# Performance work log

Hardware: AMD Instinct MI355X
Metric: run time of the kernel (lower is better)

The kernel has to match this reference:

```python
import jax, jax.numpy as jnp
import numpy as np

N_NODES = 100000
NEG_SLOPE = 0.2


def _gat_conv(x, edge_index, W, att_src, att_dst, bias):
    """Single-head PyG-style GATConv with self-loops.
    x: [N, F_in], edge_index: [2, E] (row 0 = src j, row 1 = dst i).
    """
    N = x.shape[0]
    h = x @ W  # [N, F_out]
    # add self-loops
    loop = jnp.arange(N, dtype=edge_index.dtype)
    src = jnp.concatenate([edge_index[0], loop])
    dst = jnp.concatenate([edge_index[1], loop])
    # per-node attention terms, gathered per edge
    a_s = h @ att_src  # [N]
    a_d = h @ att_dst  # [N]
    e = jax.nn.leaky_relu(a_s[src] + a_d[dst], NEG_SLOPE)  # [E+N]
    # segment softmax over incoming edges of each destination
    m = jax.ops.segment_max(e, dst, num_segments=N)  # [N]
    m = jnp.where(jnp.isfinite(m), m, 0.0)
    p = jnp.exp(e - m[dst])
    denom = jax.ops.segment_sum(p, dst, num_segments=N)  # [N], >0 due to self-loops
    alpha = p / denom[dst]  # [E+N]
    # scatter-aggregate weighted source features
    out = jax.ops.segment_sum(h[src] * alpha[:, None], dst, num_segments=N)
    return out + bias


def setup_inputs() -> dict:
    key = jax.random.key(0)
    ks = jax.random.split(key, 12)
    F_in, H, C = 128, 64, 40
    x = jax.random.normal(ks[0], (N_NODES, F_in), dtype=jnp.float32)
    edge_index = jax.random.randint(ks[1], (2, 1600000), 0, N_NODES, dtype=jnp.int64)
    s1 = 1.0 / np.sqrt(F_in)
    s2 = 1.0 / np.sqrt(H)
    return {
        "x": x,
        "edge_index": edge_index,
        "W1": jax.random.uniform(ks[2], (F_in, H), jnp.float32, -s1, s1),
        "att_src1": jax.random.uniform(ks[3], (H,), jnp.float32, -s2, s2),
        "att_dst1": jax.random.uniform(ks[4], (H,), jnp.float32, -s2, s2),
        "b1": jnp.zeros((H,), jnp.float32),
        "W2": jax.random.uniform(ks[5], (H, C), jnp.float32, -s2, s2),
        "att_src2": jax.random.uniform(ks[6], (C,), jnp.float32, -1.0 / np.sqrt(C), 1.0 / np.sqrt(C)),
        "att_dst2": jax.random.uniform(ks[7], (C,), jnp.float32, -1.0 / np.sqrt(C), 1.0 / np.sqrt(C)),
        "b2": jnp.zeros((C,), jnp.float32),
    }


def reference(x, edge_index, W1, att_src1, att_dst1, b1, W2, att_src2, att_dst2, b2):
    h = _gat_conv(x, edge_index, W1, att_src1, att_dst1, b1)
    h = jax.nn.relu(h)
    # dropout is identity in eval mode
    out = _gat_conv(h, edge_index, W2, att_src2, att_dst2, b2)
    return out
```

## Files before the change

kernel.cpp:

```cpp
#include <hip/hip_runtime.h>
#include <math.h>


#define NEG_SLOPE 0.2f
#define BIN_SHIFT 8
#define BIN_NODES 256
#define MAXBINS   512
#define CAPB      4864
#define K1_CHUNK  4096
#define MAXDEG    128
#define AGG_STRIDE 132
#define XS1 136
#define RTS 72

typedef _Float16 h4_t __attribute__((ext_vector_type(4)));
typedef _Float16 h8_t __attribute__((ext_vector_type(8)));
typedef float    f16x_t __attribute__((ext_vector_type(16)));
typedef float    f4_t  __attribute__((ext_vector_type(4)));

__device__ __forceinline__ float lrelu(float v) {
    return v > 0.f ? v : NEG_SLOPE * v;
}

__global__ __launch_bounds__(256) void prep_kernel(
    const float* __restrict__ W1, const float* __restrict__ W2,
    const float* __restrict__ as1, const float* __restrict__ ad1,
    const float* __restrict__ as2, const float* __restrict__ ad2,
    _Float16* __restrict__ w1f, _Float16* __restrict__ w2g,
    float* __restrict__ u1, float* __restrict__ v1,
    int* __restrict__ bin_cursor)
{
    const int tid = threadIdx.x;
    if (blockIdx.x == 0) {
        for (int j = tid; j < MAXBINS; j += 256) bin_cursor[j] = 0;
        for (int i = tid; i < 8192; i += 256) {
            int j = i & 7, l = (i >> 3) & 63, q = i >> 9;
            int kc = q & 7, ch = q >> 3;
            int n = ch * 32 + (l & 31);
            int k = (l >> 5) * 8 + kc * 16 + j;
            w1f[i] = (_Float16)W1[k * 64 + n];
        }
        if (tid < 128) {
            float su = 0.f, sv = 0.f;
            for (int n = 0; n < 64; ++n) {
                float w = W1[tid * 64 + n];
                su += w * as1[n];
                sv += w * ad1[n];
            }
            u1[tid] = su; v1[tid] = sv;
        }
    } else {
        __shared__ float u2l[64], v2l[64];
        if (tid < 64) {
            float su = 0.f, sv = 0.f;
            for (int n = 0; n < 40; ++n) {
                float w = W2[tid * 40 + n];
                su += w * as2[n];
                sv += w * ad2[n];
            }
            u2l[tid] = su; v2l[tid] = sv;
        }
        __syncthreads();
        for (int i = tid; i < 3072; i += 256) {
            int j = i & 7, l = (i >> 3) & 63, q = i >> 9;
            int kk = q & 1, cb = q >> 1;
            int n = cb * 16 + (l & 15);
            int k = kk * 32 + (l >> 4) * 8 + j;
            _Float16 o = (_Float16)0.f;
            if (n < 40)       o = (_Float16)W2[k * 40 + n];
            else if (n == 40) o = (_Float16)u2l[k];
            else if (n == 41) o = (_Float16)v2l[k];
            w2g[i] = o;
        }
    }
}

__global__ __launch_bounds__(256) void gemm1_bin_kernel(
    const float* __restrict__ x, const _Float16* __restrict__ w1f,
    const float* __restrict__ u1, const float* __restrict__ v1,
    _Float16* __restrict__ h, float* __restrict__ as_, float* __restrict__ ad_,
    int N, int gb,
    const int* __restrict__ src, const int* __restrict__ dst, int E, int nbins,
    int* __restrict__ bin_cursor, int* __restrict__ binned)
{
    __shared__ __align__(16) char smem[18432];
    const int tid = threadIdx.x;

    if (blockIdx.x < gb) {
        _Float16* Xs = (_Float16*)smem;
        float*    Us = (float*)(smem + 17408);
        float*    Vs = (float*)(smem + 17920);
        const int lane = tid & 63;
        const int w = tid >> 6;
        const int rh = w >> 1, ch = w & 1;
        const long rowbase = (long)blockIdx.x * 64;

        {
            const float4* X4 = (const float4*)x;
            const long gmax = (long)N * 32;
#pragma unroll
            for (int i = 0; i < 8; ++i) {
                int f = tid + i * 256;
                int row = f >> 5, c4 = f & 31;
                long gi = (rowbase + row) * 32 + c4;
                float4 v = (gi < gmax) ? X4[gi] : make_float4(0.f, 0.f, 0.f, 0.f);
                h4_t hv;
                hv.x = (_Float16)v.x; hv.y = (_Float16)v.y;
                hv.z = (_Float16)v.z; hv.w = (_Float16)v.w;
                *(h4_t*)&Xs[row * XS1 + c4 * 4] = hv;
            }
        }
        if (tid < 128) Us[tid] = u1[tid];
        else { int t = tid - 128; Vs[t] = v1[t]; }
        __syncthreads();

        {
            const int arow = tid >> 2, apart = tid & 3;
            const _Float16* xr = &Xs[arow * XS1 + apart * 32];
            float ps = 0.f, pd = 0.f;
#pragma unroll
            for (int k = 0; k < 32; k += 4) {
                h4_t xv = *(const h4_t*)(xr + k);
                float4 uu = *(const float4*)&Us[apart * 32 + k];
                float4 vv = *(const float4*)&Vs[apart * 32 + k];
                float x0 = (float)xv.x, x1 = (float)xv.y, x2 = (float)xv.z, x3 = (float)xv.w;
                ps += x0 * uu.x + x1 * uu.y + x2 * uu.z + x3 * uu.w;
                pd += x0 * vv.x + x1 * vv.y + x2 * vv.z + x3 * vv.w;
            }
            ps += __shfl_xor(ps, 1); ps += __shfl_xor(ps, 2);
            pd += __shfl_xor(pd, 1); pd += __shfl_xor(pd, 2);
            if (apart == 0 && rowbase + arow < N) {
                as_[rowbase + arow] = ps;
                ad_[rowbase + arow] = pd;
            }
        }

        const int m = lane & 31, khalf = lane >> 5;
        const _Float16* ax = &Xs[(rh * 32 + m) * XS1 + khalf * 8];
        const h8_t* bF = (const h8_t*)w1f + ch * 8 * 64 + lane;

        f16x_t acc = {};
#pragma unroll
        for (int kc = 0; kc < 8; ++kc) {
            h8_t a = *(const h8_t*)(ax + kc * 16);
            h8_t b = bF[kc * 64];
            acc = __builtin_amdgcn_mfma_f32_32x32x16_f16(a, b, acc, 0, 0, 0);
        }

        const int col = ch * 32 + m;
#pragma unroll
        for (int r = 0; r < 16; ++r) {
            int rowl = (r & 3) + 8 * (r >> 2) + 4 * khalf;
            long grow = rowbase + rh * 32 + rowl;
            if (grow < N) h[grow * 64 + col] = (_Float16)acc[r];
        }
    } else {
        int* hist = (int*)smem;
        int* base = (int*)(smem + 2048);
        int* lcur = (int*)(smem + 4096);
        const int e0 = (blockIdx.x - gb) * K1_CHUNK;

        int sreg[16], dreg[16];
#pragma unroll
        for (int k = 0; k < 16; ++k) {
            int e = e0 + tid + k * 256;
            bool ok = e < E;
            dreg[k] = ok ? dst[e] : -1;
            sreg[k] = ok ? src[e] : 0;
        }

        for (int j = tid; j < nbins; j += 256) hist[j] = 0;
        __syncthreads();
#pragma unroll
        for (int k = 0; k < 16; ++k)
            if (dreg[k] >= 0) atomicAdd(&hist[dreg[k] >> BIN_SHIFT], 1);
        __syncthreads();
        for (int j = tid; j < nbins; j += 256) {
            int c = hist[j];
            base[j] = (c > 0) ? atomicAdd(&bin_cursor[j], c) : 0;
            lcur[j] = 0;
        }
        __syncthreads();
#pragma unroll
        for (int k = 0; k < 16; ++k) {
            if (dreg[k] >= 0) {
                int b = dreg[k] >> BIN_SHIFT;
                int o = atomicAdd(&lcur[b], 1);
                int pos = base[b] + o;
                if (pos < CAPB)
                    binned[b * CAPB + pos] =
                        (sreg[k] << BIN_SHIFT) | (dreg[k] & (BIN_NODES - 1));
            }
        }
    }
}

__global__ __launch_bounds__(512) void fine_kernel(
    const int* __restrict__ bin_cursor, const int* __restrict__ binned,
    int* __restrict__ csr, int* __restrict__ rowptr, int N, int nbins)
{
    __shared__ int a[MAXBINS];
    __shared__ int nh[BIN_NODES];
    __shared__ int cur[BIN_NODES];
    __shared__ int lbuf[CAPB];
    __shared__ int sb[2];
    const int b = blockIdx.x;
    const int tid = threadIdx.x;

    int v = (tid < nbins) ? min(bin_cursor[tid], CAPB) : 0;
    a[tid] = v;
    __syncthreads();
#pragma unroll
    for (int ofs = 1; ofs < MAXBINS; ofs <<= 1) {
        int t = (tid >= ofs) ? a[tid - ofs] : 0;
        __syncthreads();
        a[tid] += t;
        __syncthreads();
    }
    if (tid == 0) {
        sb[0] = (b > 0) ? a[b - 1] : 0;
        sb[1] = a[nbins - 1];
    }

    const int cnt = min(bin_cursor[b], CAPB);
    const int nn = min(BIN_NODES, N - b * BIN_NODES);
    const int* __restrict__ brec = binned + (long)b * CAPB;

    if (tid < BIN_NODES) nh[tid] = 0;
    __syncthreads();

    for (int k = tid; k < cnt; k += 512) {
        atomicAdd(&nh[brec[k] & (BIN_NODES - 1)], 1);
    }
    __syncthreads();

    int hv = (tid < BIN_NODES) ? nh[tid] : 0;
#pragma unroll
    for (int ofs = 1; ofs < BIN_NODES; ofs <<= 1) {
        int t = (tid >= ofs && tid < BIN_NODES) ? nh[tid - ofs] : 0;
        __syncthreads();
        if (tid < BIN_NODES) nh[tid] += t;
        __syncthreads();
    }
    const int binbase = sb[0];
    if (tid < BIN_NODES) {
        int excl = nh[tid] - hv;
        if (tid < nn) rowptr[b * BIN_NODES + tid] = binbase + excl;
        cur[tid] = excl;
    }
    if (b == nbins - 1 && tid == 0) rowptr[N] = sb[1];
    __syncthreads();

    for (int k = tid; k < cnt; k += 512) {
        int rec = brec[k];
        int pos = atomicAdd(&cur[rec & (BIN_NODES - 1)], 1);
        lbuf[pos] = rec >> BIN_SHIFT;
    }
    __syncthreads();
    for (int t = tid; t < cnt; t += 512) {
        csr[binbase + t] = lbuf[t];
    }
}

__global__ __launch_bounds__(256) void agg1_fused_kernel(
    const _Float16* __restrict__ h, const float* __restrict__ as_,
    const float* __restrict__ ad_, const int* __restrict__ rowptr,
    const int* __restrict__ csr, const float* __restrict__ b1,
    const _Float16* __restrict__ w2g,
    _Float16* __restrict__ h2, float* __restrict__ as2, float* __restrict__ ad2,
    int N)
{
    __shared__ __align__(16) int      Ss[16 * AGG_STRIDE];
    __shared__ __align__(16) float    Ps[16 * AGG_STRIDE];
    __shared__ __align__(16) _Float16 Rt[16 * RTS];
    const int tid = threadIdx.x;
    const int dl  = tid >> 4;
    const int sub = tid & 15;
    const long blockbase = (long)blockIdx.x * 16;
    const long i = blockbase + dl;
    const bool alive = (i < N);

    int r0 = 0, deg = 0;
    if (alive) {
        r0 = rowptr[i];
        deg = rowptr[i + 1] - r0;
        if (deg > MAXDEG) deg = MAXDEG;
    }
    const float adi    = alive ? ad_[i] : 0.f;
    const float e_self = alive ? lrelu(as_[i] + adi) : 0.f;

    int*   __restrict__ sp = &Ss[dl * AGG_STRIDE];
    float* __restrict__ pp = &Ps[dl * AGG_STRIDE];

    float psum = 0.f;
    for (int c = sub; c < deg; c += 16) {
        int s = csr[r0 + c];
        float p = __expf(lrelu(as_[s] + adi));
        sp[c] = s;
        pp[c] = p;
        psum += p;
    }
#pragma unroll
    for (int off = 1; off < 16; off <<= 1) psum += __shfl_xor(psum, off);
    const float p_self = __expf(e_self);
    const float inv = 1.f / (psum + p_self);

    const int col = sub * 4;
    float4 acc = make_float4(0.f, 0.f, 0.f, 0.f);

    int k = 0;
    for (; k + 8 <= deg; k += 8) {
        int4   s0 = *(const int4*)&sp[k];
        int4   s1 = *(const int4*)&sp[k + 4];
        float4 p0 = *(const float4*)&pp[k];
        float4 p1 = *(const float4*)&pp[k + 4];
        h4_t hA = *(const h4_t*)&h[(long)s0.x * 64 + col];
        h4_t hB = *(const h4_t*)&h[(long)s0.y * 64 + col];
        h4_t hC = *(const h4_t*)&h[(long)s0.z * 64 + col];
        h4_t hD = *(const h4_t*)&h[(long)s0.w * 64 + col];
        h4_t hE = *(const h4_t*)&h[(long)s1.x * 64 + col];
        h4_t hF = *(const h4_t*)&h[(long)s1.y * 64 + col];
        h4_t hG = *(const h4_t*)&h[(long)s1.z * 64 + col];
        h4_t hH = *(const h4_t*)&h[(long)s1.w * 64 + col];
        acc.x += (float)hA.x * p0.x + (float)hB.x * p0.y + (float)hC.x * p0.z + (float)hD.x * p0.w
               + (float)hE.x * p1.x + (float)hF.x * p1.y + (float)hG.x * p1.z + (float)hH.x * p1.w;
        acc.y += (float)hA.y * p0.x + (float)hB.y * p0.y + (float)hC.y * p0.z + (float)hD.y * p0.w
               + (float)hE.y * p1.x + (float)hF.y * p1.y + (float)hG.y * p1.z + (float)hH.y * p1.w;
        acc.z += (float)hA.z * p0.x + (float)hB.z * p0.y + (float)hC.z * p0.z + (float)hD.z * p0.w
               + (float)hE.z * p1.x + (float)hF.z * p1.y + (float)hG.z * p1.z + (float)hH.z * p1.w;
        acc.w += (float)hA.w * p0.x + (float)hB.w * p0.y + (float)hC.w * p0.z + (float)hD.w * p0.w
               + (float)hE.w * p1.x + (float)hF.w * p1.y + (float)hG.w * p1.z + (float)hH.w * p1.w;
    }
    for (; k + 4 <= deg; k += 4) {
        int4   s0 = *(const int4*)&sp[k];
        float4 p0 = *(const float4*)&pp[k];
        h4_t hA = *(const h4_t*)&h[(long)s0.x * 64 + col];
        h4_t hB = *(const h4_t*)&h[(long)s0.y * 64 + col];
        h4_t hC = *(const h4_t*)&h[(long)s0.z * 64 + col];
        h4_t hD = *(const h4_t*)&h[(long)s0.w * 64 + col];
        acc.x += (float)hA.x * p0.x + (float)hB.x * p0.y + (float)hC.x * p0.z + (float)hD.x * p0.w;
        acc.y += (float)hA.y * p0.x + (float)hB.y * p0.y + (float)hC.y * p0.z + (float)hD.y * p0.w;
        acc.z += (float)hA.z * p0.x + (float)hB.z * p0.y + (float)hC.z * p0.z + (float)hD.z * p0.w;
        acc.w += (float)hA.w * p0.x + (float)hB.w * p0.y + (float)hC.w * p0.z + (float)hD.w * p0.w;
    }
    for (; k < deg; ++k) {
        int   s = sp[k];
        float p = pp[k];
        h4_t hv = *(const h4_t*)&h[(long)s * 64 + col];
        acc.x += (float)hv.x * p; acc.y += (float)hv.y * p;
        acc.z += (float)hv.z * p; acc.w += (float)hv.w * p;
    }

    h4_t hv = {};
    if (alive) hv = *(const h4_t*)&h[i * 64 + col];
    float4 bv = *(const float4*)&b1[col];
    h4_t rt;
    rt.x = (_Float16)fmaxf((acc.x + (float)hv.x * p_self) * inv + bv.x, 0.f);
    rt.y = (_Float16)fmaxf((acc.y + (float)hv.y * p_self) * inv + bv.y, 0.f);
    rt.z = (_Float16)fmaxf((acc.z + (float)hv.z * p_self) * inv + bv.z, 0.f);
    rt.w = (_Float16)fmaxf((acc.w + (float)hv.w * p_self) * inv + bv.w, 0.f);
    *(h4_t*)&Rt[dl * RTS + sub * 4] = rt;
    __syncthreads();

    const int w = tid >> 6, lane = tid & 63;
    if (w < 3) {
        const int arow = lane & 15, kq = lane >> 4;
        f4_t c = {};
#pragma unroll
        for (int kk = 0; kk < 2; ++kk) {
            h8_t a = *(const h8_t*)&Rt[arow * RTS + kk * 32 + kq * 8];
            h8_t b = ((const h8_t*)w2g)[(w * 2 + kk) * 64 + lane];
            c = __builtin_amdgcn_mfma_f32_16x16x32_f16(a, b, c, 0, 0, 0);
        }
        const int ocol = w * 16 + (lane & 15);
#pragma unroll
        for (int r = 0; r < 4; ++r) {
            int orow = (lane >> 4) * 4 + r;
            long gi = blockbase + orow;
            if (gi < N) {
                float v = c[r];
                if (ocol < 40)       h2[gi * 64 + ocol] = (_Float16)v;
                else if (ocol == 40) as2[gi] = v;
                else if (ocol == 41) ad2[gi] = v;
            }
        }
    }
}

template<int F, int LD, typename OT>
__global__ __launch_bounds__(256) void aggregate_kernel(
    const _Float16* __restrict__ h, const float* __restrict__ as_,
    const float* __restrict__ ad_, const int* __restrict__ rowptr,
    const int* __restrict__ csr, const float* __restrict__ bias,
    OT* __restrict__ out, int N)
{
    __shared__ __align__(16) int   Ss[16 * AGG_STRIDE];
    __shared__ __align__(16) float Ps[16 * AGG_STRIDE];
    const int tid = threadIdx.x;
    const int dl  = tid >> 4;
    const int sub = tid & 15;
    const int i = blockIdx.x * 16 + dl;
    const bool alive = (i < N);

    int r0 = 0, deg = 0;
    if (alive) {
        r0 = rowptr[i];
        deg = rowptr[i + 1] - r0;
        if (deg > MAXDEG) deg = MAXDEG;
    }
    const float adi    = alive ? ad_[i] : 0.f;
    const float e_self = alive ? lrelu(as_[i] + adi) : 0.f;

    int*   __restrict__ sp = &Ss[dl * AGG_STRIDE];
    float* __restrict__ pp = &Ps[dl * AGG_STRIDE];

    float psum = 0.f;
    for (int c = sub; c < deg; c += 16) {
        int s = csr[r0 + c];
        float p = __expf(lrelu(as_[s] + adi));
        sp[c] = s;
        pp[c] = p;
        psum += p;
    }
#pragma unroll
    for (int off = 1; off < 16; off <<= 1) psum += __shfl_xor(psum, off);
    const float p_self = __expf(e_self);
    const float inv = 1.f / (psum + p_self);

    const bool act = (sub * 4 < F);
    const int  col = act ? sub * 4 : 0;
    float4 acc = make_float4(0.f, 0.f, 0.f, 0.f);

    int k = 0;
    for (; k + 8 <= deg; k += 8) {
        int4   s0 = *(const int4*)&sp[k];
        int4   s1 = *(const int4*)&sp[k + 4];
        float4 p0 = *(const float4*)&pp[k];
        float4 p1 = *(const float4*)&pp[k + 4];
        if (act) {
            h4_t hA = *(const h4_t*)&h[(long)s0.x * LD + col];
            h4_t hB = *(const h4_t*)&h[(long)s0.y * LD + col];
            h4_t hC = *(const h4_t*)&h[(long)s0.z * LD + col];
            h4_t hD = *(const h4_t*)&h[(long)s0.w * LD + col];
            h4_t hE = *(const h4_t*)&h[(long)s1.x * LD + col];
            h4_t hF = *(const h4_t*)&h[(long)s1.y * LD + col];
            h4_t hG = *(const h4_t*)&h[(long)s1.z * LD + col];
            h4_t hH = *(const h4_t*)&h[(long)s1.w * LD + col];
            acc.x += (float)hA.x * p0.x + (float)hB.x * p0.y + (float)hC.x * p0.z + (float)hD.x * p0.w
                   + (float)hE.x * p1.x + (float)hF.x * p1.y + (float)hG.x * p1.z + (float)hH.x * p1.w;
            acc.y += (float)hA.y * p0.x + (float)hB.y * p0.y + (float)hC.y * p0.z + (float)hD.y * p0.w
                   + (float)hE.y * p1.x + (float)hF.y * p1.y + (float)hG.y * p1.z + (float)hH.y * p1.w;
            acc.z += (float)hA.z * p0.x + (float)hB.z * p0.y + (float)hC.z * p0.z + (float)hD.z * p0.w
                   + (float)hE.z * p1.x + (float)hF.z * p1.y + (float)hG.z * p1.z + (float)hH.z * p1.w;
            acc.w += (float)hA.w * p0.x + (float)hB.w * p0.y + (float)hC.w * p0.z + (float)hD.w * p0.w
                   + (float)hE.w * p1.x + (float)hF.w * p1.y + (float)hG.w * p1.z + (float)hH.w * p1.w;
        }
    }
    for (; k + 4 <= deg; k += 4) {
        int4   s0 = *(const int4*)&sp[k];
        float4 p0 = *(const float4*)&pp[k];
        if (act) {
            h4_t hA = *(const h4_t*)&h[(long)s0.x * LD + col];
            h4_t hB = *(const h4_t*)&h[(long)s0.y * LD + col];
            h4_t hC = *(const h4_t*)&h[(long)s0.z * LD + col];
            h4_t hD = *(const h4_t*)&h[(long)s0.w * LD + col];
            acc.x += (float)hA.x * p0.x + (float)hB.x * p0.y + (float)hC.x * p0.z + (float)hD.x * p0.w;
            acc.y += (float)hA.y * p0.x + (float)hB.y * p0.y + (float)hC.y * p0.z + (float)hD.y * p0.w;
            acc.z += (float)hA.z * p0.x + (float)hB.z * p0.y + (float)hC.z * p0.z + (float)hD.z * p0.w;
            acc.w += (float)hA.w * p0.x + (float)hB.w * p0.y + (float)hC.w * p0.z + (float)hD.w * p0.w;
        }
    }
    for (; k < deg; ++k) {
        int   s = sp[k];
        float p = pp[k];
        if (act) {
            h4_t hv = *(const h4_t*)&h[(long)s * LD + col];
            acc.x += (float)hv.x * p; acc.y += (float)hv.y * p;
            acc.z += (float)hv.z * p; acc.w += (float)hv.w * p;
        }
    }

    if (alive && act) {
        h4_t hv = *(const h4_t*)&h[(long)i * LD + col];
        float4 bv = *(const float4*)&bias[col];
        float ox = (acc.x + (float)hv.x * p_self) * inv + bv.x;
        float oy = (acc.y + (float)hv.y * p_self) * inv + bv.y;
        float oz = (acc.z + (float)hv.z * p_self) * inv + bv.z;
        float ow = (acc.w + (float)hv.w * p_self) * inv + bv.w;
        if constexpr (sizeof(OT) == 4) {
            float4 o = make_float4(ox, oy, oz, ow);
            *(float4*)&out[(long)i * F + col] = o;
        } else {
            h4_t o;
            o.x = (_Float16)ox; o.y = (_Float16)oy;
            o.z = (_Float16)oz; o.w = (_Float16)ow;
            *(h4_t*)&out[(long)i * F + col] = o;
        }
    }
}

extern "C" void kernel_launch(void* const* d_in, const int* in_sizes, int n_in,
                              void* d_out, int out_size, void* d_ws, size_t ws_size,
                              hipStream_t stream) {
    const float* x    = (const float*)d_in[0];
    const int*   ei   = (const int*)d_in[1];
    const float* W1   = (const float*)d_in[2];
    const float* at_s1= (const float*)d_in[3];
    const float* at_d1= (const float*)d_in[4];
    const float* b1   = (const float*)d_in[5];
    const float* W2   = (const float*)d_in[6];
    const float* at_s2= (const float*)d_in[7];
    const float* at_d2= (const float*)d_in[8];
    const float* b2   = (const float*)d_in[9];
    float* out = (float*)d_out;

    const int N = in_sizes[0] / 128;
    const int E = in_sizes[1] / 2;
    const int nbins = (N + BIN_NODES - 1) >> BIN_SHIFT;

    char* p = (char*)d_ws;
    auto carve = [&](size_t bytes) -> void* {
        void* r = (void*)p;
        p += (bytes + 255) & ~(size_t)255;
        return r;
    };
    int*       bin_cursor = (int*)      carve((size_t)MAXBINS * 4);
    int*       binned     = (int*)      carve((size_t)nbins * CAPB * 4);
    int*       csr        = (int*)      carve((size_t)E * 4);
    int*       rowptr     = (int*)      carve((size_t)(N + 1) * 4);
    _Float16*  w1f        = (_Float16*) carve((size_t)8192 * 2);
    _Float16*  w2g        = (_Float16*) carve((size_t)3072 * 2);
    float*     u1         = (float*)    carve((size_t)128 * 4);
    float*     v1         = (float*)    carve((size_t)128 * 4);
    _Float16*  h1         = (_Float16*) carve((size_t)N * 64 * 2);
    _Float16*  h2         = (_Float16*) carve((size_t)N * 64 * 2);
    float*     asn        = (float*)    carve((size_t)N * 4);
    float*     adn        = (float*)    carve((size_t)N * 4);
    float*     as2n       = (float*)    carve((size_t)N * 4);
    float*     ad2n       = (float*)    carve((size_t)N * 4);

    prep_kernel<<<2, 256, 0, stream>>>(W1, W2, at_s1, at_d1, at_s2, at_d2,
                                       w1f, w2g, u1, v1, bin_cursor);

    const int gb = (N + 63) / 64;
    const int bb = (E + K1_CHUNK - 1) / K1_CHUNK;
    gemm1_bin_kernel<<<gb + bb, 256, 0, stream>>>(
        x, w1f, u1, v1, h1, asn, adn, N, gb,
        ei, ei + E, E, nbins, bin_cursor, binned);

    fine_kernel<<<nbins, 512, 0, stream>>>(bin_cursor, binned, csr, rowptr, N, nbins);

    agg1_fused_kernel<<<(N + 15) / 16, 256, 0, stream>>>(
        h1, asn, adn, rowptr, csr, b1, w2g, h2, as2n, ad2n, N);

    aggregate_kernel<40, 64, float><<<(N + 15) / 16, 256, 0, stream>>>(
        h2, as2n, ad2n, rowptr, csr, b2, out, N);
}
```

Baseline: 219.7 us.

## Stage binned edges in shared memory before writing them to global bins

The edge-binning branch now halves the chunk per block and runs a shared-memory prefix scan over the per-bin histogram. Each block writes its records to a local shared buffer grouped by bin, then copies each bin's run to global memory contiguously. This replaces scattered per-edge global writes with grouped writes and doubles the number of binning blocks for more parallelism. The cost is extra barriers for the scan and a serial per-thread copy loop that can be uneven across bins.

```diff
diff --git a/kernel.cpp b/kernel.cpp
--- a/kernel.cpp
+++ b/kernel.cpp
@@ -7,7 +7,7 @@
 #define BIN_NODES 256
 #define MAXBINS   512
 #define CAPB      4864
-#define K1_CHUNK  4096
+#define K1_CHUNK  2048
 #define MAXDEG    128
 #define AGG_STRIDE 132
 #define XS1 136
@@ -155,41 +155,68 @@
             if (grow < N) h[grow * 64 + col] = (_Float16)acc[r];
         }
     } else {
-        int* hist = (int*)smem;
-        int* base = (int*)(smem + 2048);
-        int* lcur = (int*)(smem + 4096);
+        int* hist  = (int*)smem;
+        int* base  = (int*)(smem + 2048);
+        int* lbase = (int*)(smem + 4096);
+        int* lcur  = (int*)(smem + 6144);
+        int* lrec  = (int*)(smem + 8192);
         const int e0 = (blockIdx.x - gb) * K1_CHUNK;
 
-        int sreg[16], dreg[16];
-#pragma unroll
-        for (int k = 0; k < 16; ++k) {
+        int sreg[8], dreg[8];
+#pragma unroll
+        for (int k = 0; k < 8; ++k) {
             int e = e0 + tid + k * 256;
             bool ok = e < E;
             dreg[k] = ok ? dst[e] : -1;
             sreg[k] = ok ? src[e] : 0;
         }
 
-        for (int j = tid; j < nbins; j += 256) hist[j] = 0;
-        __syncthreads();
-#pragma unroll
-        for (int k = 0; k < 16; ++k)
+        for (int j = tid; j < MAXBINS; j += 256) hist[j] = 0;
+        __syncthreads();
+#pragma unroll
+        for (int k = 0; k < 8; ++k)
             if (dreg[k] >= 0) atomicAdd(&hist[dreg[k] >> BIN_SHIFT], 1);
         __syncthreads();
-        for (int j = tid; j < nbins; j += 256) {
+
+        const int h0 = hist[2 * tid], h1 = hist[2 * tid + 1];
+        const int s2 = h0 + h1;
+        lcur[tid] = s2;
+        __syncthreads();
+#pragma unroll
+        for (int ofs = 1; ofs < 256; ofs <<= 1) {
+            int t = (tid >= ofs) ? lcur[tid - ofs] : 0;
+            __syncthreads();
+            lcur[tid] += t;
+            __syncthreads();
+        }
+        const int excl = lcur[tid] - s2;
+        lbase[2 * tid]     = excl;
+        lbase[2 * tid + 1] = excl + h0;
+        __syncthreads();
+
+        for (int j = tid; j < MAXBINS; j += 256) {
             int c = hist[j];
             base[j] = (c > 0) ? atomicAdd(&bin_cursor[j], c) : 0;
             lcur[j] = 0;
         }
         __syncthreads();
-#pragma unroll
-        for (int k = 0; k < 16; ++k) {
+
+#pragma unroll
+        for (int k = 0; k < 8; ++k) {
             if (dreg[k] >= 0) {
                 int b = dreg[k] >> BIN_SHIFT;
                 int o = atomicAdd(&lcur[b], 1);
-                int pos = base[b] + o;
-                if (pos < CAPB)
-                    binned[b * CAPB + pos] =
-                        (sreg[k] << BIN_SHIFT) | (dreg[k] & (BIN_NODES - 1));
+                lrec[lbase[b] + o] =
+                    (sreg[k] << BIN_SHIFT) | (dreg[k] & (BIN_NODES - 1));
+            }
+        }
+        __syncthreads();
+
+        for (int j = tid; j < nbins; j += 256) {
+            int c = hist[j], g0 = base[j], lb = lbase[j];
+            long gbb = (long)j * CAPB + g0;
+            for (int t = 0; t < c; ++t) {
+                if (g0 + t < CAPB) binned[gbb + t] = lrec[lb + t];
             }
         }
     }
```

New measurement: 224.1 us. 1.02x slower.
